# Kernel tuning notes

Hardware: AMD Instinct MI355X
Metric: run time of the kernel (lower is better)

## Reference

```python
import jax, jax.numpy as jnp
import numpy as np

N_NODES = 100000
N_EDGES = 1600000
D_IN = 128
D_OUT = 128


def setup_inputs() -> dict:
    key = jax.random.key(0)
    k = jax.random.split(key, 6)
    x = jax.random.normal(k[0], (N_NODES, D_IN), dtype=jnp.float32)
    edge_src = jax.random.randint(k[1], (N_EDGES,), 0, N_NODES, dtype=jnp.int64)
    edge_dst = jax.random.randint(k[2], (N_EDGES,), 0, N_NODES, dtype=jnp.int64)
    edge_weight = jax.random.uniform(k[3], (N_EDGES,), dtype=jnp.float32)
    # xavier-uniform-ish init for the two projection matrices
    lim = float(np.sqrt(6.0 / (D_IN + D_OUT)))
    W_nbrs = jax.random.uniform(k[4], (D_IN, D_OUT), minval=-lim, maxval=lim, dtype=jnp.float32)
    W_self = jax.random.uniform(k[5], (D_IN, D_OUT), minval=-lim, maxval=lim, dtype=jnp.float32)
    bias = jnp.zeros((D_OUT,), dtype=jnp.float32)
    return {"x": x, "edge_src": edge_src, "edge_dst": edge_dst,
            "edge_weight": edge_weight, "W_nbrs": W_nbrs, "W_self": W_self,
            "bias": bias}


def reference(x, edge_src, edge_dst, edge_weight, W_nbrs, W_self, bias):
    # y = x @ W_nbrs  (dense projection)
    y = x @ W_nbrs                                   # [N, D_OUT]
    # spmm(adj, y): out[i] = sum_{(j->i) in E} w_ij * y[j]
    msgs = edge_weight[:, None] * y[edge_src]        # [E, D_OUT]
    agg = jax.ops.segment_sum(msgs, edge_dst, num_segments=x.shape[0])
    # self transform + bias
    return agg + x @ W_self + bias
```

## Files before the change

### kernel.cpp

```cpp
#include <hip/hip_runtime.h>
#include <hip/hip_bf16.h>

#define D 128

typedef __bf16 bf16x8 __attribute__((ext_vector_type(8)));
typedef unsigned short u16x8 __attribute__((ext_vector_type(8)));
typedef float f32x4 __attribute__((ext_vector_type(4)));

__device__ __forceinline__ unsigned short f2bf(float f) {
    unsigned u = __float_as_uint(f);
    u += 0x7FFFu + ((u >> 16) & 1u);
    return (unsigned short)(u >> 16);
}
__device__ __forceinline__ float bf2f(unsigned u16) {
    return __uint_as_float(u16 << 16);
}

__global__ void k_build_wt(const float* __restrict__ Wn, const float* __restrict__ Ws,
                           unsigned short* __restrict__ WTs,
                           int* __restrict__ cnt, int N) {
    int g = blockIdx.x * blockDim.x + threadIdx.x;
    int k = g >> 8;
    int c = g & 255;
    float v = (c < 128) ? Wn[k * 128 + c] : Ws[k * 128 + (c - 128)];
    int chunk = k >> 3;
    WTs[c * 128 + (((chunk ^ (c & 15)) << 3) | (k & 7))] = f2bf(v);
    for (int i = g; i < N; i += 32768) cnt[i] = 0;
}

__global__ __launch_bounds__(256) void k1_gemm_y_rank(
    const float* __restrict__ x, const unsigned short* __restrict__ WTs, int N,
    unsigned short* __restrict__ y,
    const int* __restrict__ edst, int E,
    int* __restrict__ cnt, int* __restrict__ rank) {
    __shared__ unsigned short sm[128 * 128];
    int b = blockIdx.x;
    int tid = threadIdx.x;
    if (b & 1) {
        int e0 = (b >> 1) * 1024 + tid * 4;
        if (e0 + 3 < E) {
            int4 d4 = *(const int4*)(edst + e0);
            int r0 = atomicAdd(&cnt[d4.x], 1);
            int r1 = atomicAdd(&cnt[d4.y], 1);
            int r2 = atomicAdd(&cnt[d4.z], 1);
            int r3 = atomicAdd(&cnt[d4.w], 1);
            *(int4*)(rank + e0) = make_int4(r0, r1, r2, r3);
        } else {
            for (int e = e0; e < E && e < e0 + 4; ++e)
                rank[e] = atomicAdd(&cnt[edst[e]], 1);
        }
        return;
    }
    int gb = b >> 1;
    int brow = gb * 64;
    if (brow >= N) return;
    int w = tid >> 6, l = tid & 63;
    int row0 = brow + w * 16;
    int c15 = l & 15;
    int kgrp = l >> 4;
    const uint4* gs = (const uint4*)WTs;
    uint4* ss = (uint4*)sm;
    uint4 st[8];
    #pragma unroll
    for (int r = 0; r < 8; ++r) st[r] = gs[r * 256 + tid];
    int arow = row0 + c15;
    bool avalid = (arow < N);
    const float* xr = x + (size_t)arow * D;
    bf16x8 afrag[4];
    #pragma unroll
    for (int ks = 0; ks < 4; ++ks) {
        int k0 = ks * 32 + kgrp * 8;
        float4 a0, a1;
        if (avalid) { a0 = *(const float4*)(xr + k0); a1 = *(const float4*)(xr + k0 + 4); }
        else { a0 = make_float4(0.f, 0.f, 0.f, 0.f); a1 = a0; }
        bf16x8 f;
        f[0] = (__bf16)a0.x; f[1] = (__bf16)a0.y; f[2] = (__bf16)a0.z; f[3] = (__bf16)a0.w;
        f[4] = (__bf16)a1.x; f[5] = (__bf16)a1.y; f[6] = (__bf16)a1.z; f[7] = (__bf16)a1.w;
        afrag[ks] = f;
    }
    #pragma unroll
    for (int r = 0; r < 8; ++r) ss[r * 256 + tid] = st[r];
    __syncthreads();
    f32x4 acc[8];
    #pragma unroll
    for (int nt = 0; nt < 8; ++nt) {
        int c = nt * 16 + c15;
        f32x4 a = {0.f, 0.f, 0.f, 0.f};
        #pragma unroll
        for (int ks = 0; ks < 4; ++ks) {
            int chunk = ks * 4 + kgrp;
            const bf16x8* bp = (const bf16x8*)(sm + c * 128 + ((chunk ^ c15) << 3));
            a = __builtin_amdgcn_mfma_f32_16x16x32_bf16(afrag[ks], *bp, a, 0, 0, 0);
        }
        acc[nt] = a;
    }
    int orow = row0 + kgrp * 4;
    #pragma unroll
    for (int j = 0; j < 4; ++j) {
        int r = orow + j;
        if (r < N) {
            u16x8 f;
            #pragma unroll
            for (int nt = 0; nt < 8; ++nt) f[nt] = f2bf(acc[nt][j]);
            *(u16x8*)(y + (size_t)r * D + c15 * 8) = f;
        }
    }
}

__global__ void k_scanA(const int* __restrict__ cnt, int N,
                        int* __restrict__ ofs, int* __restrict__ bsum) {
    __shared__ int lds[1024];
    int t = threadIdx.x, i = blockIdx.x * 1024 + t;
    int v = (i < N) ? cnt[i] : 0;
    lds[t] = v; __syncthreads();
    for (int d = 1; d < 1024; d <<= 1) {
        int x = (t >= d) ? lds[t - d] : 0; __syncthreads();
        lds[t] += x; __syncthreads();
    }
    if (i < N) ofs[i] = lds[t] - v;
    if (t == 1023) bsum[blockIdx.x] = lds[t];
}

__global__ void k_scanB(int* __restrict__ bsum, int NB) {
    __shared__ int lds[128];
    int t = threadIdx.x;
    int v = (t < NB) ? bsum[t] : 0;
    lds[t] = v; __syncthreads();
    for (int d = 1; d < 128; d <<= 1) {
        int x = (t >= d) ? lds[t - d] : 0; __syncthreads();
        lds[t] += x; __syncthreads();
    }
    if (t < NB) bsum[t] = lds[t] - v;
}

__global__ __launch_bounds__(256) void k2_gemm_self_fill(
    const float* __restrict__ x, const unsigned short* __restrict__ WTs,
    const float* __restrict__ bias, int N,
    float* __restrict__ out,
    const int* __restrict__ src, const int* __restrict__ dst,
    const float* __restrict__ ew, const int* __restrict__ rank, int E,
    const int* __restrict__ ofs, const int* __restrict__ bsum,
    uint2* __restrict__ sorted) {
    __shared__ unsigned short sm[128 * 128];
    int b = blockIdx.x;
    int tid = threadIdx.x;
    if (b & 1) {
        int e0 = (b >> 1) * 1024 + tid * 4;
        if (e0 + 3 < E) {
            int4 d4 = *(const int4*)(dst + e0);
            int4 s4 = *(const int4*)(src + e0);
            float4 w4 = *(const float4*)(ew + e0);
            int4 r4 = *(const int4*)(rank + e0);
            sorted[ofs[d4.x] + bsum[d4.x >> 10] + r4.x] = make_uint2((unsigned)s4.x, __float_as_uint(w4.x));
            sorted[ofs[d4.y] + bsum[d4.y >> 10] + r4.y] = make_uint2((unsigned)s4.y, __float_as_uint(w4.y));
            sorted[ofs[d4.z] + bsum[d4.z >> 10] + r4.z] = make_uint2((unsigned)s4.z, __float_as_uint(w4.z));
            sorted[ofs[d4.w] + bsum[d4.w >> 10] + r4.w] = make_uint2((unsigned)s4.w, __float_as_uint(w4.w));
        } else {
            for (int e = e0; e < E && e < e0 + 4; ++e) {
                int d = dst[e];
                sorted[ofs[d] + bsum[d >> 10] + rank[e]] =
                    make_uint2((unsigned)src[e], __float_as_uint(ew[e]));
            }
        }
        return;
    }
    int gb = b >> 1;
    int brow = gb * 64;
    if (brow >= N) return;
    int w = tid >> 6, l = tid & 63;
    int row0 = brow + w * 16;
    int c15 = l & 15;
    int kgrp = l >> 4;
    const uint4* gs = (const uint4*)WTs;
    uint4* ss = (uint4*)sm;
    uint4 st[8];
    #pragma unroll
    for (int r = 0; r < 8; ++r) st[r] = gs[2048 + r * 256 + tid];
    int arow = row0 + c15;
    bool avalid = (arow < N);
    const float* xr = x + (size_t)arow * D;
    bf16x8 afrag[4];
    #pragma unroll
    for (int ks = 0; ks < 4; ++ks) {
        int k0 = ks * 32 + kgrp * 8;
        float4 a0, a1;
        if (avalid) { a0 = *(const float4*)(xr + k0); a1 = *(const float4*)(xr + k0 + 4); }
        else { a0 = make_float4(0.f, 0.f, 0.f, 0.f); a1 = a0; }
        bf16x8 f;
        f[0] = (__bf16)a0.x; f[1] = (__bf16)a0.y; f[2] = (__bf16)a0.z; f[3] = (__bf16)a0.w;
        f[4] = (__bf16)a1.x; f[5] = (__bf16)a1.y; f[6] = (__bf16)a1.z; f[7] = (__bf16)a1.w;
        afrag[ks] = f;
    }
    #pragma unroll
    for (int r = 0; r < 8; ++r) ss[r * 256 + tid] = st[r];
    __syncthreads();
    f32x4 acc[8];
    #pragma unroll
    for (int nt = 0; nt < 8; ++nt) {
        int c = nt * 16 + c15;
        f32x4 a = {0.f, 0.f, 0.f, 0.f};
        #pragma unroll
        for (int ks = 0; ks < 4; ++ks) {
            int chunk = ks * 4 + kgrp;
            const bf16x8* bp = (const bf16x8*)(sm + c * 128 + ((chunk ^ c15) << 3));
            a = __builtin_amdgcn_mfma_f32_16x16x32_bf16(afrag[ks], *bp, a, 0, 0, 0);
        }
        acc[nt] = a;
    }
    float bv[8];
    #pragma unroll
    for (int nt = 0; nt < 8; ++nt) bv[nt] = bias[nt * 16 + c15];
    int orow = row0 + kgrp * 4;
    #pragma unroll
    for (int j = 0; j < 4; ++j) {
        int r = orow + j;
        if (r < N) {
            float4 s0 = make_float4(acc[0][j] + bv[0], acc[1][j] + bv[1],
                                    acc[2][j] + bv[2], acc[3][j] + bv[3]);
            float4 s1 = make_float4(acc[4][j] + bv[4], acc[5][j] + bv[5],
                                    acc[6][j] + bv[6], acc[7][j] + bv[7]);
            float4* op = (float4*)(out + (size_t)r * D + c15 * 8);
            op[0] = s0; op[1] = s1;
        }
    }
}

__global__ __launch_bounds__(256) void k_agg(
    const unsigned short* __restrict__ y, const uint2* __restrict__ sorted,
    const int* __restrict__ ofs, const int* __restrict__ bsum,
    const int* __restrict__ cnt, int N,
    float* __restrict__ out) {
    int w = threadIdx.x >> 6, l = threadIdx.x & 63;
    int node = blockIdx.x * 4 + w;
    if (node >= N) return;
    int s = ofs[node] + bsum[node >> 10], n = cnt[node];
    int g = l >> 4, li = l & 15;
    float4 s0, s1;
    if (l < 16) {
        const float4* spf = (const float4*)(out + (size_t)node * D + li * 8);
        s0 = spf[0]; s1 = spf[1];
    }
    const uint2* sp = sorted + s;
    float a0 = 0.f, a1 = 0.f, a2 = 0.f, a3 = 0.f;
    float a4 = 0.f, a5 = 0.f, a6 = 0.f, a7 = 0.f;
    int j = g;
    for (; j + 4 < n; j += 8) {
        uint2 pa = sp[j];
        uint2 pb = sp[j + 4];
        uint4 va = *(const uint4*)(y + (size_t)pa.x * D + li * 8);
        uint4 vb = *(const uint4*)(y + (size_t)pb.x * D + li * 8);
        float wa = __uint_as_float(pa.y), wb = __uint_as_float(pb.y);
        a0 += wa * bf2f(va.x & 0xFFFFu); a1 += wa * bf2f(va.x >> 16);
        a2 += wa * bf2f(va.y & 0xFFFFu); a3 += wa * bf2f(va.y >> 16);
        a4 += wa * bf2f(va.z & 0xFFFFu); a5 += wa * bf2f(va.z >> 16);
        a6 += wa * bf2f(va.w & 0xFFFFu); a7 += wa * bf2f(va.w >> 16);
        a0 += wb * bf2f(vb.x & 0xFFFFu); a1 += wb * bf2f(vb.x >> 16);
        a2 += wb * bf2f(vb.y & 0xFFFFu); a3 += wb * bf2f(vb.y >> 16);
        a4 += wb * bf2f(vb.z & 0xFFFFu); a5 += wb * bf2f(vb.z >> 16);
        a6 += wb * bf2f(vb.w & 0xFFFFu); a7 += wb * bf2f(vb.w >> 16);
    }
    if (j < n) {
        uint2 p = sp[j];
        uint4 v = *(const uint4*)(y + (size_t)p.x * D + li * 8);
        float wt = __uint_as_float(p.y);
        a0 += wt * bf2f(v.x & 0xFFFFu); a1 += wt * bf2f(v.x >> 16);
        a2 += wt * bf2f(v.y & 0xFFFFu); a3 += wt * bf2f(v.y >> 16);
        a4 += wt * bf2f(v.z & 0xFFFFu); a5 += wt * bf2f(v.z >> 16);
        a6 += wt * bf2f(v.w & 0xFFFFu); a7 += wt * bf2f(v.w >> 16);
    }
    a0 += __shfl_xor(a0, 16, 64); a1 += __shfl_xor(a1, 16, 64);
    a2 += __shfl_xor(a2, 16, 64); a3 += __shfl_xor(a3, 16, 64);
    a4 += __shfl_xor(a4, 16, 64); a5 += __shfl_xor(a5, 16, 64);
    a6 += __shfl_xor(a6, 16, 64); a7 += __shfl_xor(a7, 16, 64);
    a0 += __shfl_xor(a0, 32, 64); a1 += __shfl_xor(a1, 32, 64);
    a2 += __shfl_xor(a2, 32, 64); a3 += __shfl_xor(a3, 32, 64);
    a4 += __shfl_xor(a4, 32, 64); a5 += __shfl_xor(a5, 32, 64);
    a6 += __shfl_xor(a6, 32, 64); a7 += __shfl_xor(a7, 32, 64);
    if (l < 16) {
        float* op = out + (size_t)node * D + li;
        op[0]   = a0 + s0.x; op[16]  = a1 + s0.y;
        op[32]  = a2 + s0.z; op[48]  = a3 + s0.w;
        op[64]  = a4 + s1.x; op[80]  = a5 + s1.y;
        op[96]  = a6 + s1.z; op[112] = a7 + s1.w;
    }
}

extern "C" void kernel_launch(void* const* d_in, const int* in_sizes, int n_in,
                              void* d_out, int out_size, void* d_ws, size_t ws_size,
                              hipStream_t stream) {
    const float* x    = (const float*)d_in[0];
    const int*   esrc = (const int*)d_in[1];
    const int*   edst = (const int*)d_in[2];
    const float* ew   = (const float*)d_in[3];
    const float* Wn   = (const float*)d_in[4];
    const float* Wsf  = (const float*)d_in[5];
    const float* bias = (const float*)d_in[6];
    float* out = (float*)d_out;
    int N = in_sizes[0] / D;
    int E = in_sizes[1];

    char* ws = (char*)d_ws;
    size_t off = 0;
    unsigned short* WTs = (unsigned short*)(ws + off); off += 256 * 128 * sizeof(unsigned short);
    unsigned short* yb  = (unsigned short*)(ws + off); off += (size_t)N * D * sizeof(unsigned short);
    off = (off + 255) & ~(size_t)255;
    int* cnt  = (int*)(ws + off); off += (size_t)N * 4; off = (off + 255) & ~(size_t)255;
    int* ofs  = (int*)(ws + off); off += (size_t)N * 4; off = (off + 255) & ~(size_t)255;
    int* bsum = (int*)(ws + off); off += 1024;
    int* rank = (int*)(ws + off); off += (size_t)E * 4; off = (off + 255) & ~(size_t)255;
    uint2* sorted = (uint2*)(ws + off); off += (size_t)E * 8;

    k_build_wt<<<128, 256, 0, stream>>>(Wn, Wsf, WTs, cnt, N);

    int GB = (N + 63) / 64;
    int RB = (E + 1023) / 1024;
    int M1 = (GB > RB ? GB : RB);
    k1_gemm_y_rank<<<M1 * 2, 256, 0, stream>>>(x, WTs, N, yb, edst, E, cnt, rank);

    int NB = (N + 1023) / 1024;
    k_scanA<<<NB, 1024, 0, stream>>>(cnt, N, ofs, bsum);
    k_scanB<<<1, 128, 0, stream>>>(bsum, NB);

    k2_gemm_self_fill<<<M1 * 2, 256, 0, stream>>>(x, WTs, bias, N, out,
                                                  esrc, edst, ew, rank, E,
                                                  ofs, bsum, sorted);

    k_agg<<<(N + 3) / 4, 256, 0, stream>>>(yb, sorted, ofs, bsum, cnt, N, out);
}
```

Baseline: 296.6 us.

## Interleave edge counting/scatter with GEMM inside each block, shuffle-based scan, deeper agg unroll

The two fused kernels stop splitting blocks into alternating GEMM-only and edge-only roles. Each block now does both: it issues its edge loads and atomics or index lookups in between staging the GEMM tile and running the MFMAs, so their latency overlaps with matrix work, and the grid is halved. The block scan now uses wavefront shuffles instead of a 10-step LDS Hillis-Steele loop, and the aggregation loop handles four neighbours per iteration for more memory-level parallelism. The risks are higher register pressure from the combined paths, and a `__syncthreads` that sits inside a branch. That branch is uniform across the block because it depends only on the block index.

```diff
diff --git a/kernel.cpp b/kernel.cpp
--- a/kernel.cpp
+++ b/kernel.cpp
@@ -36,89 +36,111 @@
     __shared__ unsigned short sm[128 * 128];
     int b = blockIdx.x;
     int tid = threadIdx.x;
-    if (b & 1) {
-        int e0 = (b >> 1) * 1024 + tid * 4;
-        if (e0 + 3 < E) {
-            int4 d4 = *(const int4*)(edst + e0);
-            int r0 = atomicAdd(&cnt[d4.x], 1);
-            int r1 = atomicAdd(&cnt[d4.y], 1);
-            int r2 = atomicAdd(&cnt[d4.z], 1);
-            int r3 = atomicAdd(&cnt[d4.w], 1);
-            *(int4*)(rank + e0) = make_int4(r0, r1, r2, r3);
-        } else {
-            for (int e = e0; e < E && e < e0 + 4; ++e)
-                rank[e] = atomicAdd(&cnt[edst[e]], 1);
-        }
-        return;
-    }
-    int gb = b >> 1;
-    int brow = gb * 64;
-    if (brow >= N) return;
+    int e0 = b * 1024 + tid * 4;
+    bool efull = (e0 + 3 < E);
+    bool etail = !efull && (e0 < E);
+    int4 d4 = make_int4(0, 0, 0, 0);
+    if (efull) d4 = *(const int4*)(edst + e0);
+
+    int brow = b * 64;
+    bool gvalid = (brow < N);
     int w = tid >> 6, l = tid & 63;
-    int row0 = brow + w * 16;
     int c15 = l & 15;
     int kgrp = l >> 4;
-    const uint4* gs = (const uint4*)WTs;
-    uint4* ss = (uint4*)sm;
-    uint4 st[8];
-    #pragma unroll
-    for (int r = 0; r < 8; ++r) st[r] = gs[r * 256 + tid];
-    int arow = row0 + c15;
-    bool avalid = (arow < N);
-    const float* xr = x + (size_t)arow * D;
     bf16x8 afrag[4];
-    #pragma unroll
-    for (int ks = 0; ks < 4; ++ks) {
-        int k0 = ks * 32 + kgrp * 8;
-        float4 a0, a1;
-        if (avalid) { a0 = *(const float4*)(xr + k0); a1 = *(const float4*)(xr + k0 + 4); }
-        else { a0 = make_float4(0.f, 0.f, 0.f, 0.f); a1 = a0; }
-        bf16x8 f;
-        f[0] = (__bf16)a0.x; f[1] = (__bf16)a0.y; f[2] = (__bf16)a0.z; f[3] = (__bf16)a0.w;
-        f[4] = (__bf16)a1.x; f[5] = (__bf16)a1.y; f[6] = (__bf16)a1.z; f[7] = (__bf16)a1.w;
-        afrag[ks] = f;
-    }
-    #pragma unroll
-    for (int r = 0; r < 8; ++r) ss[r * 256 + tid] = st[r];
-    __syncthreads();
-    f32x4 acc[8];
-    #pragma unroll
-    for (int nt = 0; nt < 8; ++nt) {
-        int c = nt * 16 + c15;
-        f32x4 a = {0.f, 0.f, 0.f, 0.f};
+    if (gvalid) {
+        const uint4* gs = (const uint4*)WTs;
+        uint4* ss = (uint4*)sm;
+        uint4 st[8];
+        #pragma unroll
+        for (int r = 0; r < 8; ++r) st[r] = gs[r * 256 + tid];
+        int row0 = brow + w * 16;
+        int arow = row0 + c15;
+        bool avalid = (arow < N);
+        const float* xr = x + (size_t)arow * D;
         #pragma unroll
         for (int ks = 0; ks < 4; ++ks) {
-            int chunk = ks * 4 + kgrp;
-            const bf16x8* bp = (const bf16x8*)(sm + c * 128 + ((chunk ^ c15) << 3));
-            a = __builtin_amdgcn_mfma_f32_16x16x32_bf16(afrag[ks], *bp, a, 0, 0, 0);
-        }
-        acc[nt] = a;
-    }
-    int orow = row0 + kgrp * 4;
-    #pragma unroll
-    for (int j = 0; j < 4; ++j) {
-        int r = orow + j;
-        if (r < N) {
-            u16x8 f;
+            int k0 = ks * 32 + kgrp * 8;
+            float4 a0, a1;
+            if (avalid) { a0 = *(const float4*)(xr + k0); a1 = *(const float4*)(xr + k0 + 4); }
+            else { a0 = make_float4(0.f, 0.f, 0.f, 0.f); a1 = a0; }
+            bf16x8 f;
+            f[0] = (__bf16)a0.x; f[1] = (__bf16)a0.y; f[2] = (__bf16)a0.z; f[3] = (__bf16)a0.w;
+            f[4] = (__bf16)a1.x; f[5] = (__bf16)a1.y; f[6] = (__bf16)a1.z; f[7] = (__bf16)a1.w;
+            afrag[ks] = f;
+        }
+        #pragma unroll
+        for (int r = 0; r < 8; ++r) ss[r * 256 + tid] = st[r];
+        __syncthreads();
+    }
+    int r0 = 0, r1 = 0, r2 = 0, r3 = 0;
+    if (efull) {
+        r0 = atomicAdd(&cnt[d4.x], 1);
+        r1 = atomicAdd(&cnt[d4.y], 1);
+        r2 = atomicAdd(&cnt[d4.z], 1);
+        r3 = atomicAdd(&cnt[d4.w], 1);
+    }
+    if (gvalid) {
+        f32x4 acc[8];
+        #pragma unroll
+        for (int nt = 0; nt < 8; ++nt) {
+            int c = nt * 16 + c15;
+            f32x4 a = {0.f, 0.f, 0.f, 0.f};
             #pragma unroll
-            for (int nt = 0; nt < 8; ++nt) f[nt] = f2bf(acc[nt][j]);
-            *(u16x8*)(y + (size_t)r * D + c15 * 8) = f;
-        }
+            for (int ks = 0; ks < 4; ++ks) {
+                int chunk = ks * 4 + kgrp;
+                const bf16x8* bp = (const bf16x8*)(sm + c * 128 + ((chunk ^ c15) << 3));
+                a = __builtin_amdgcn_mfma_f32_16x16x32_bf16(afrag[ks], *bp, a, 0, 0, 0);
+            }
+            acc[nt] = a;
+        }
+        int orow = brow + w * 16 + kgrp * 4;
+        #pragma unroll
+        for (int j = 0; j < 4; ++j) {
+            int r = orow + j;
+            if (r < N) {
+                u16x8 f;
+                #pragma unroll
+                for (int nt = 0; nt < 8; ++nt) f[nt] = f2bf(acc[nt][j]);
+                *(u16x8*)(y + (size_t)r * D + c15 * 8) = f;
+            }
+        }
+    }
+    if (efull) {
+        *(int4*)(rank + e0) = make_int4(r0, r1, r2, r3);
+    } else if (etail) {
+        for (int e = e0; e < E; ++e) rank[e] = atomicAdd(&cnt[edst[e]], 1);
     }
 }
 
 __global__ void k_scanA(const int* __restrict__ cnt, int N,
                         int* __restrict__ ofs, int* __restrict__ bsum) {
-    __shared__ int lds[1024];
+    __shared__ int ws[16];
     int t = threadIdx.x, i = blockIdx.x * 1024 + t;
     int v = (i < N) ? cnt[i] : 0;
-    lds[t] = v; __syncthreads();
-    for (int d = 1; d < 1024; d <<= 1) {
-        int x = (t >= d) ? lds[t - d] : 0; __syncthreads();
-        lds[t] += x; __syncthreads();
-    }
-    if (i < N) ofs[i] = lds[t] - v;
-    if (t == 1023) bsum[blockIdx.x] = lds[t];
+    int s = v;
+    #pragma unroll
+    for (int d = 1; d < 64; d <<= 1) {
+        int xp = __shfl_up(s, d, 64);
+        if ((t & 63) >= d) s += xp;
+    }
+    int wid = t >> 6;
+    if ((t & 63) == 63) ws[wid] = s;
+    __syncthreads();
+    if (wid == 0) {
+        int wv = (t < 16) ? ws[t] : 0;
+        #pragma unroll
+        for (int d = 1; d < 16; d <<= 1) {
+            int xp = __shfl_up(wv, d, 64);
+            if (t >= d && t < 16) wv += xp;
+        }
+        if (t < 16) ws[t] = wv;
+    }
+    __syncthreads();
+    int base = (wid > 0) ? ws[wid - 1] : 0;
+    int incl = s + base;
+    if (i < N) ofs[i] = incl - v;
+    if (t == 1023) bsum[blockIdx.x] = incl;
 }
 
 __global__ void k_scanB(int* __restrict__ bsum, int NB) {
@@ -144,83 +166,95 @@
     __shared__ unsigned short sm[128 * 128];
     int b = blockIdx.x;
     int tid = threadIdx.x;
-    if (b & 1) {
-        int e0 = (b >> 1) * 1024 + tid * 4;
-        if (e0 + 3 < E) {
-            int4 d4 = *(const int4*)(dst + e0);
-            int4 s4 = *(const int4*)(src + e0);
-            float4 w4 = *(const float4*)(ew + e0);
-            int4 r4 = *(const int4*)(rank + e0);
-            sorted[ofs[d4.x] + bsum[d4.x >> 10] + r4.x] = make_uint2((unsigned)s4.x, __float_as_uint(w4.x));
-            sorted[ofs[d4.y] + bsum[d4.y >> 10] + r4.y] = make_uint2((unsigned)s4.y, __float_as_uint(w4.y));
-            sorted[ofs[d4.z] + bsum[d4.z >> 10] + r4.z] = make_uint2((unsigned)s4.z, __float_as_uint(w4.z));
-            sorted[ofs[d4.w] + bsum[d4.w >> 10] + r4.w] = make_uint2((unsigned)s4.w, __float_as_uint(w4.w));
-        } else {
-            for (int e = e0; e < E && e < e0 + 4; ++e) {
-                int d = dst[e];
-                sorted[ofs[d] + bsum[d >> 10] + rank[e]] =
-                    make_uint2((unsigned)src[e], __float_as_uint(ew[e]));
-            }
-        }
-        return;
-    }
-    int gb = b >> 1;
-    int brow = gb * 64;
-    if (brow >= N) return;
+    int e0 = b * 1024 + tid * 4;
+    bool efull = (e0 + 3 < E);
+    bool etail = !efull && (e0 < E);
+    int4 d4 = make_int4(0,0,0,0), s4 = make_int4(0,0,0,0), r4 = make_int4(0,0,0,0);
+    float4 w4 = make_float4(0.f,0.f,0.f,0.f);
+    if (efull) {
+        d4 = *(const int4*)(dst + e0);
+        s4 = *(const int4*)(src + e0);
+        w4 = *(const float4*)(ew + e0);
+        r4 = *(const int4*)(rank + e0);
+    }
+    int brow = b * 64;
+    bool gvalid = (brow < N);
     int w = tid >> 6, l = tid & 63;
-    int row0 = brow + w * 16;
     int c15 = l & 15;
     int kgrp = l >> 4;
-    const uint4* gs = (const uint4*)WTs;
-    uint4* ss = (uint4*)sm;
-    uint4 st[8];
-    #pragma unroll
-    for (int r = 0; r < 8; ++r) st[r] = gs[2048 + r * 256 + tid];
-    int arow = row0 + c15;
-    bool avalid = (arow < N);
-    const float* xr = x + (size_t)arow * D;
     bf16x8 afrag[4];
-    #pragma unroll
-    for (int ks = 0; ks < 4; ++ks) {
-        int k0 = ks * 32 + kgrp * 8;
-        float4 a0, a1;
-        if (avalid) { a0 = *(const float4*)(xr + k0); a1 = *(const float4*)(xr + k0 + 4); }
-        else { a0 = make_float4(0.f, 0.f, 0.f, 0.f); a1 = a0; }
-        bf16x8 f;
-        f[0] = (__bf16)a0.x; f[1] = (__bf16)a0.y; f[2] = (__bf16)a0.z; f[3] = (__bf16)a0.w;
-        f[4] = (__bf16)a1.x; f[5] = (__bf16)a1.y; f[6] = (__bf16)a1.z; f[7] = (__bf16)a1.w;
-        afrag[ks] = f;
-    }
-    #pragma unroll
-    for (int r = 0; r < 8; ++r) ss[r * 256 + tid] = st[r];
-    __syncthreads();
-    f32x4 acc[8];
-    #pragma unroll
-    for (int nt = 0; nt < 8; ++nt) {
-        int c = nt * 16 + c15;
-        f32x4 a = {0.f, 0.f, 0.f, 0.f};
+    if (gvalid) {
+        const uint4* gs = (const uint4*)WTs;
+        uint4* ss = (uint4*)sm;
+        uint4 st[8];
+        #pragma unroll
+        for (int r = 0; r < 8; ++r) st[r] = gs[2048 + r * 256 + tid];
+        int arow = brow + w * 16 + c15;
+        bool avalid = (arow < N);
+        const float* xr = x + (size_t)arow * D;
         #pragma unroll
         for (int ks = 0; ks < 4; ++ks) {
-            int chunk = ks * 4 + kgrp;
-            const bf16x8* bp = (const bf16x8*)(sm + c * 128 + ((chunk ^ c15) << 3));
-            a = __builtin_amdgcn_mfma_f32_16x16x32_bf16(afrag[ks], *bp, a, 0, 0, 0);
-        }
-        acc[nt] = a;
-    }
-    float bv[8];
-    #pragma unroll
-    for (int nt = 0; nt < 8; ++nt) bv[nt] = bias[nt * 16 + c15];
-    int orow = row0 + kgrp * 4;
-    #pragma unroll
-    for (int j = 0; j < 4; ++j) {
-        int r = orow + j;
-        if (r < N) {
-            float4 s0 = make_float4(acc[0][j] + bv[0], acc[1][j] + bv[1],
-                                    acc[2][j] + bv[2], acc[3][j] + bv[3]);
-            float4 s1 = make_float4(acc[4][j] + bv[4], acc[5][j] + bv[5],
-                                    acc[6][j] + bv[6], acc[7][j] + bv[7]);
-            float4* op = (float4*)(out + (size_t)r * D + c15 * 8);
-            op[0] = s0; op[1] = s1;
+            int k0 = ks * 32 + kgrp * 8;
+            float4 a0, a1;
+            if (avalid) { a0 = *(const float4*)(xr + k0); a1 = *(const float4*)(xr + k0 + 4); }
+            else { a0 = make_float4(0.f, 0.f, 0.f, 0.f); a1 = a0; }
+            bf16x8 f;
+            f[0] = (__bf16)a0.x; f[1] = (__bf16)a0.y; f[2] = (__bf16)a0.z; f[3] = (__bf16)a0.w;
+            f[4] = (__bf16)a1.x; f[5] = (__bf16)a1.y; f[6] = (__bf16)a1.z; f[7] = (__bf16)a1.w;
+            afrag[ks] = f;
+        }
+        #pragma unroll
+        for (int r = 0; r < 8; ++r) ss[r * 256 + tid] = st[r];
+        __syncthreads();
+    }
+    int p0 = 0, p1 = 0, p2 = 0, p3 = 0;
+    if (efull) {
+        p0 = ofs[d4.x] + bsum[d4.x >> 10] + r4.x;
+        p1 = ofs[d4.y] + bsum[d4.y >> 10] + r4.y;
+        p2 = ofs[d4.z] + bsum[d4.z >> 10] + r4.z;
+        p3 = ofs[d4.w] + bsum[d4.w >> 10] + r4.w;
+    }
+    if (gvalid) {
+        f32x4 acc[8];
+        #pragma unroll
+        for (int nt = 0; nt < 8; ++nt) {
+            int c = nt * 16 + c15;
+            f32x4 a = {0.f, 0.f, 0.f, 0.f};
+            #pragma unroll
+            for (int ks = 0; ks < 4; ++ks) {
+                int chunk = ks * 4 + kgrp;
+                const bf16x8* bp = (const bf16x8*)(sm + c * 128 + ((chunk ^ c15) << 3));
+                a = __builtin_amdgcn_mfma_f32_16x16x32_bf16(afrag[ks], *bp, a, 0, 0, 0);
+            }
+            acc[nt] = a;
+        }
+        float bv[8];
+        #pragma unroll
+        for (int nt = 0; nt < 8; ++nt) bv[nt] = bias[nt * 16 + c15];
+        int orow = brow + w * 16 + kgrp * 4;
+        #pragma unroll
+        for (int j = 0; j < 4; ++j) {
+            int r = orow + j;
+            if (r < N) {
+                float4 s0 = make_float4(acc[0][j] + bv[0], acc[1][j] + bv[1],
+                                        acc[2][j] + bv[2], acc[3][j] + bv[3]);
+                float4 s1 = make_float4(acc[4][j] + bv[4], acc[5][j] + bv[5],
+                                        acc[6][j] + bv[6], acc[7][j] + bv[7]);
+                float4* op = (float4*)(out + (size_t)r * D + c15 * 8);
+                op[0] = s0; op[1] = s1;
+            }
+        }
+    }
+    if (efull) {
+        sorted[p0] = make_uint2((unsigned)s4.x, __float_as_uint(w4.x));
+        sorted[p1] = make_uint2((unsigned)s4.y, __float_as_uint(w4.y));
+        sorted[p2] = make_uint2((unsigned)s4.z, __float_as_uint(w4.z));
+        sorted[p3] = make_uint2((unsigned)s4.w, __float_as_uint(w4.w));
+    } else if (etail) {
+        for (int e = e0; e < E; ++e) {
+            int d = dst[e];
+            sorted[ofs[d] + bsum[d >> 10] + rank[e]] =
+                make_uint2((unsigned)src[e], __float_as_uint(ew[e]));
         }
     }
 }
@@ -244,22 +278,35 @@
     float a0 = 0.f, a1 = 0.f, a2 = 0.f, a3 = 0.f;
     float a4 = 0.f, a5 = 0.f, a6 = 0.f, a7 = 0.f;
     int j = g;
-    for (; j + 4 < n; j += 8) {
-        uint2 pa = sp[j];
-        uint2 pb = sp[j + 4];
-        uint4 va = *(const uint4*)(y + (size_t)pa.x * D + li * 8);
-        uint4 vb = *(const uint4*)(y + (size_t)pb.x * D + li * 8);
-        float wa = __uint_as_float(pa.y), wb = __uint_as_float(pb.y);
-        a0 += wa * bf2f(va.x & 0xFFFFu); a1 += wa * bf2f(va.x >> 16);
-        a2 += wa * bf2f(va.y & 0xFFFFu); a3 += wa * bf2f(va.y >> 16);
-        a4 += wa * bf2f(va.z & 0xFFFFu); a5 += wa * bf2f(va.z >> 16);
-        a6 += wa * bf2f(va.w & 0xFFFFu); a7 += wa * bf2f(va.w >> 16);
-        a0 += wb * bf2f(vb.x & 0xFFFFu); a1 += wb * bf2f(vb.x >> 16);
-        a2 += wb * bf2f(vb.y & 0xFFFFu); a3 += wb * bf2f(vb.y >> 16);
-        a4 += wb * bf2f(vb.z & 0xFFFFu); a5 += wb * bf2f(vb.z >> 16);
-        a6 += wb * bf2f(vb.w & 0xFFFFu); a7 += wb * bf2f(vb.w >> 16);
-    }
-    if (j < n) {
+    for (; j + 12 < n; j += 16) {
+        uint2 p0 = sp[j];
+        uint2 p1 = sp[j + 4];
+        uint2 p2 = sp[j + 8];
+        uint2 p3 = sp[j + 12];
+        uint4 v0 = *(const uint4*)(y + (size_t)p0.x * D + li * 8);
+        uint4 v1 = *(const uint4*)(y + (size_t)p1.x * D + li * 8);
+        uint4 v2 = *(const uint4*)(y + (size_t)p2.x * D + li * 8);
+        uint4 v3 = *(const uint4*)(y + (size_t)p3.x * D + li * 8);
+        float w0 = __uint_as_float(p0.y), w1 = __uint_as_float(p1.y);
+        float w2 = __uint_as_float(p2.y), w3 = __uint_as_float(p3.y);
+        a0 += w0 * bf2f(v0.x & 0xFFFFu); a1 += w0 * bf2f(v0.x >> 16);
+        a2 += w0 * bf2f(v0.y & 0xFFFFu); a3 += w0 * bf2f(v0.y >> 16);
+        a4 += w0 * bf2f(v0.z & 0xFFFFu); a5 += w0 * bf2f(v0.z >> 16);
+        a6 += w0 * bf2f(v0.w & 0xFFFFu); a7 += w0 * bf2f(v0.w >> 16);
+        a0 += w1 * bf2f(v1.x & 0xFFFFu); a1 += w1 * bf2f(v1.x >> 16);
+        a2 += w1 * bf2f(v1.y & 0xFFFFu); a3 += w1 * bf2f(v1.y >> 16);
+        a4 += w1 * bf2f(v1.z & 0xFFFFu); a5 += w1 * bf2f(v1.z >> 16);
+        a6 += w1 * bf2f(v1.w & 0xFFFFu); a7 += w1 * bf2f(v1.w >> 16);
+        a0 += w2 * bf2f(v2.x & 0xFFFFu); a1 += w2 * bf2f(v2.x >> 16);
+        a2 += w2 * bf2f(v2.y & 0xFFFFu); a3 += w2 * bf2f(v2.y >> 16);
+        a4 += w2 * bf2f(v2.z & 0xFFFFu); a5 += w2 * bf2f(v2.z >> 16);
+        a6 += w2 * bf2f(v2.w & 0xFFFFu); a7 += w2 * bf2f(v2.w >> 16);
+        a0 += w3 * bf2f(v3.x & 0xFFFFu); a1 += w3 * bf2f(v3.x >> 16);
+        a2 += w3 * bf2f(v3.y & 0xFFFFu); a3 += w3 * bf2f(v3.y >> 16);
+        a4 += w3 * bf2f(v3.z & 0xFFFFu); a5 += w3 * bf2f(v3.z >> 16);
+        a6 += w3 * bf2f(v3.w & 0xFFFFu); a7 += w3 * bf2f(v3.w >> 16);
+    }
+    for (; j < n; j += 4) {
         uint2 p = sp[j];
         uint4 v = *(const uint4*)(y + (size_t)p.x * D + li * 8);
         float wt = __uint_as_float(p.y);
@@ -314,16 +361,16 @@
 
     int GB = (N + 63) / 64;
     int RB = (E + 1023) / 1024;
-    int M1 = (GB > RB ? GB : RB);
-    k1_gemm_y_rank<<<M1 * 2, 256, 0, stream>>>(x, WTs, N, yb, edst, E, cnt, rank);
+    int M = (GB > RB ? GB : RB);
+    k1_gemm_y_rank<<<M, 256, 0, stream>>>(x, WTs, N, yb, edst, E, cnt, rank);
 
     int NB = (N + 1023) / 1024;
     k_scanA<<<NB, 1024, 0, stream>>>(cnt, N, ofs, bsum);
     k_scanB<<<1, 128, 0, stream>>>(bsum, NB);
 
-    k2_gemm_self_fill<<<M1 * 2, 256, 0, stream>>>(x, WTs, bias, N, out,
-                                                  esrc, edst, ew, rank, E,
-                                                  ofs, bsum, sorted);
+    k2_gemm_self_fill<<<M, 256, 0, stream>>>(x, WTs, bias, N, out,
+                                             esrc, edst, ew, rank, E,
+                                             ofs, bsum, sorted);
 
     k_agg<<<(N + 3) / 4, 256, 0, stream>>>(yb, sorted, ofs, bsum, cnt, N, out);
 }
```

After: 303.5 us. +2.3%, slower.
